# Kernel optimization log

Measured on AMD Instinct MI355X. Metric: run time of the kernel, lower is better.

The kernel has to match this reference:

```python
import jax, jax.numpy as jnp
import numpy as np

N = 32768      # total points (8 clouds x 4096)
B = 8          # clouds in batch
D_IN = 64      # input feature dim
M = 8192       # sampled centers (ratio=0.25)
K = 32         # knn neighbors
R = 0.2        # ball radius
DIMS = [D_IN + 3, 128, 128, 256]  # edge MLP (PointNetConv local_nn)


def setup_inputs() -> dict:
    key = jax.random.key(0)
    ks = jax.random.split(key, 10)
    x = jax.random.normal(ks[0], (N, D_IN), jnp.float32)
    pos = jax.random.uniform(ks[1], (N, 3), jnp.float32)  # unit cube
    batch = jnp.repeat(jnp.arange(B, dtype=jnp.int32), N // B)
    # deterministic stand-in for torch.sort(torch.randperm(N)[:M])
    idx = jnp.sort(jax.random.permutation(ks[2], N)[:M]).astype(jnp.int32)
    params = {}
    for i in range(3):
        fan_in = DIMS[i]
        params[f"W{i+1}"] = jax.random.normal(ks[3 + 2 * i], (DIMS[i], DIMS[i + 1]), jnp.float32) / np.sqrt(fan_in)
        params[f"b{i+1}"] = jnp.zeros((DIMS[i + 1],), jnp.float32)
    return {"x": x, "pos": pos, "batch": batch, "idx": idx, **params}


def _knn_ball(pos, batch, idx, k, r):
    """Batched KNN restricted to same cloud, then radius mask (ball query)."""
    centers = pos[idx]                                   # [M, 3]
    d2 = (jnp.sum(centers ** 2, -1)[:, None]
          + jnp.sum(pos ** 2, -1)[None, :]
          - 2.0 * centers @ pos.T)                       # [M, N]
    same = batch[idx][:, None] == batch[None, :]
    d2 = jnp.where(same, d2, jnp.inf)
    neg_d2, nbr = jax.lax.top_k(-d2, k)                  # [M, K]
    valid = (-neg_d2) <= r * r                           # ball-query radius clip
    return nbr, valid


def reference(x, pos, batch, idx, W1, b1, W2, b2, W3, b3):
    nbr, valid = _knn_ball(pos, batch, idx, K, R)        # [M,K], [M,K]
    centers = pos[idx]                                   # [M, 3]
    rel = pos[nbr] - centers[:, None, :]                 # [M, K, 3]
    feat = jnp.concatenate([x[nbr], rel], axis=-1)       # [M, K, D_IN+3]
    h = jax.nn.relu(feat @ W1 + b1)
    h = jax.nn.relu(h @ W2 + b2)
    h = jax.nn.relu(h @ W3 + b3)                         # [M, K, 256]
    # max aggregation over valid neighbors (scatter-max equivalent)
    h = jnp.where(valid[:, :, None], h, -jnp.inf)
    out = jnp.max(h, axis=1)                             # [M, 256]
    return out, pos[idx], batch[idx]
```

## Files before the change

kernel.cpp:

```cpp
#include <hip/hip_runtime.h>


typedef unsigned short u16;
typedef unsigned int u32;
typedef unsigned long long u64;
typedef __bf16 bf16x8 __attribute__((ext_vector_type(8)));
typedef float floatx4 __attribute__((ext_vector_type(4)));

#define PCLOUD 4096
#define DIN    64
#define MCENT  8192
#define KNBR   32
#define CAP    448

#define OFF_LIST  0
#define OFF_HIST  14336
#define OFF_NBRL  14848
#define OFF_CNT   15360
#define OFF_CEN   15392
#define OFF_BCL   15456

__device__ inline u16 f2bf(float f) {
    u32 b = __float_as_uint(f);
    b += 0x7fffu + ((b >> 16) & 1u);
    return (u16)(b >> 16);
}
__device__ inline u32 pk2(float a, float b) { return (u32)f2bf(a) | ((u32)f2bf(b) << 16); }
__device__ inline u64 wave_min_u64(u64 v) {
    #pragma unroll
    for (int off = 32; off; off >>= 1) {
        u64 o = __shfl_xor((unsigned long long)v, off);
        if (o < v) v = o;
    }
    return v;
}
__device__ inline u64 d2key(float d2, int j) {
    u32 u = __float_as_uint(d2);
    u = (u & 0x80000000u) ? ~u : (u | 0x80000000u);
    return ((u64)u << 32) | (u32)j;
}
__device__ inline int key_bucket(u64 k) {
    u32 hi = (u32)(k >> 32);
    if (hi < 0x80000000u) return 0;
    float d2 = __uint_as_float(hi & 0x7fffffffu);
    int b = (int)(d2 * 800.0f);
    return b > 31 ? 31 : b;
}

__global__ void prep_kernel(const float* __restrict__ W1, const float* __restrict__ W2,
                            const float* __restrict__ W3, uint4* __restrict__ ws) {
    int t = blockIdx.x * 256 + threadIdx.x;
    int g = t >> 11, r = t & 2047;
    int n = r >> 4, kc = r & 15;
    const float* W; int rs, n0, krows;
    if (g == 0)      { W = W1; rs = 128; n0 = 0;   krows = 67;  }
    else if (g == 1) { W = W2; rs = 128; n0 = 0;   krows = 128; }
    else if (g == 2) { W = W3; rs = 256; n0 = 0;   krows = 128; }
    else             { W = W3; rs = 256; n0 = 128; krows = 128; }
    u16 e[8];
    #pragma unroll
    for (int j = 0; j < 8; j++) {
        int k = kc * 8 + j;
        e[j] = (k < krows) ? f2bf(W[(size_t)k * rs + n0 + n]) : (u16)0;
    }
    ws[(g << 11) + (n << 4) + (kc ^ (n & 7))] = *(const uint4*)e;
}

template <bool WS>
__device__ __forceinline__ void commitW(int s, uint4 ld, uint4* __restrict__ buf, int tid,
                                        const float* __restrict__ W1,
                                        const float* __restrict__ W2,
                                        const float* __restrict__ W3) {
    if constexpr (WS) {
        buf[tid] = ld;
    } else {
        const float* W; int rs, n0, krows;
        if (s < 8)       { W = W1; rs = 128; n0 = s * 16;        krows = 67;  }
        else if (s < 16) { W = W2; rs = 128; n0 = (s - 8) * 16;  krows = 128; }
        else             { W = W3; rs = 256; n0 = (s - 16) * 16; krows = 128; }
        int n = tid >> 4, kc = tid & 15;
        u16 e[8];
        #pragma unroll
        for (int j = 0; j < 8; j++) {
            int k = kc * 8 + j;
            e[j] = (k < krows) ? f2bf(W[(size_t)k * rs + n0 + n]) : (u16)0;
        }
        buf[(n << 4) + (kc ^ (n & 7))] = *(const uint4*)e;
    }
}

__device__ __forceinline__ void push_hit(int c, float d2, int j,
                                         int* acnt, u32* hist, u64* lists) {
    int p = atomicAdd(&acnt[c], 1);
    int bkt = (int)(d2 * 800.0f);
    bkt = bkt < 0 ? 0 : (bkt > 31 ? 31 : bkt);
    atomicAdd(&hist[c * 32 + bkt], 1u);
    if (p < CAP) lists[c * CAP + p] = d2key(d2, j);
}

template <bool WS>
__global__ __launch_bounds__(256, 4) void sa_kernel(
    const float* __restrict__ x, const float* __restrict__ pos,
    const int* __restrict__ batch, const int* __restrict__ idx,
    const float* __restrict__ W1, const float* __restrict__ b1,
    const float* __restrict__ W2, const float* __restrict__ b2,
    const float* __restrict__ W3, const float* __restrict__ b3,
    const uint4* __restrict__ ws4, float* __restrict__ out) {
    __shared__ __align__(16) char smem[40960];
    u64*  lists = (u64*)(smem + OFF_LIST);
    u32*  hist  = (u32*)(smem + OFF_HIST);
    int*  nbrl  = (int*)(smem + OFF_NBRL);
    int*  acnt  = (int*)(smem + OFF_CNT);
    int*  cnt2  = (int*)(smem + OFF_CNT + 16);
    float4* cen = (float4*)(smem + OFF_CEN);
    int*  bcls  = (int*)(smem + OFF_BCL);

    int tid = threadIdx.x, w = tid >> 6, l = tid & 63;
    int bid = blockIdx.x;
    int m0 = ((bid & 7) << 10) + ((bid >> 3) << 2);
    int m = m0 + w;
    int ic = idx[m] & (8 * PCLOUD - 1);
    float cx = pos[ic * 3], cy = pos[ic * 3 + 1], cz = pos[ic * 3 + 2];
    float sc = __fadd_rn(__fadd_rn(__fmul_rn(cx, cx), __fmul_rn(cy, cy)), __fmul_rn(cz, cz));
    int bcl = batch[ic] & 7;
    int base = bcl << 12;
    const float R2 = 0.04f;

    if (l == 0) { cen[w] = make_float4(cx, cy, cz, sc); bcls[w] = bcl; }
    if (tid < 128) hist[tid] = 0;
    if (tid < 4) { acnt[tid] = 0; cnt2[tid] = 0; }
    if (l == 1) {
        float* o1 = out + MCENT * 256;
        o1[m * 3] = cx; o1[m * 3 + 1] = cy; o1[m * 3 + 2] = cz;
        (o1 + MCENT * 3)[m] = (float)bcl;
    }
    __syncthreads();

    bool uni = (bcls[0] == bcls[1]) && (bcls[1] == bcls[2]) && (bcls[2] == bcls[3]);
    if (uni) {
        float4 cA = cen[0], cB = cen[1], cC = cen[2], cD = cen[3];
        int jb = bcls[0] << 12;
        const float* pb = pos + (size_t)jb * 3;
        #pragma unroll 4
        for (int t = tid; t < PCLOUD; t += 256) {
            float px = pb[t * 3], py = pb[t * 3 + 1], pz = pb[t * 3 + 2];
            float sp = __fadd_rn(__fadd_rn(__fmul_rn(px, px), __fmul_rn(py, py)), __fmul_rn(pz, pz));
            {
                float dt = __fadd_rn(__fadd_rn(__fmul_rn(cA.x, px), __fmul_rn(cA.y, py)), __fmul_rn(cA.z, pz));
                float d2 = __fsub_rn(__fadd_rn(cA.w, sp), __fmul_rn(2.0f, dt));
                if (d2 <= R2) push_hit(0, d2, jb + t, acnt, hist, lists);
            }
            {
                float dt = __fadd_rn(__fadd_rn(__fmul_rn(cB.x, px), __fmul_rn(cB.y, py)), __fmul_rn(cB.z, pz));
                float d2 = __fsub_rn(__fadd_rn(cB.w, sp), __fmul_rn(2.0f, dt));
                if (d2 <= R2) push_hit(1, d2, jb + t, acnt, hist, lists);
            }
            {
                float dt = __fadd_rn(__fadd_rn(__fmul_rn(cC.x, px), __fmul_rn(cC.y, py)), __fmul_rn(cC.z, pz));
                float d2 = __fsub_rn(__fadd_rn(cC.w, sp), __fmul_rn(2.0f, dt));
                if (d2 <= R2) push_hit(2, d2, jb + t, acnt, hist, lists);
            }
            {
                float dt = __fadd_rn(__fadd_rn(__fmul_rn(cD.x, px), __fmul_rn(cD.y, py)), __fmul_rn(cD.z, pz));
                float d2 = __fsub_rn(__fadd_rn(cD.w, sp), __fmul_rn(2.0f, dt));
                if (d2 <= R2) push_hit(3, d2, jb + t, acnt, hist, lists);
            }
        }
    } else {
        for (int t = l; t < PCLOUD; t += 64) {
            int j = base + t;
            float px = pos[j * 3], py = pos[j * 3 + 1], pz = pos[j * 3 + 2];
            float sp = __fadd_rn(__fadd_rn(__fmul_rn(px, px), __fmul_rn(py, py)), __fmul_rn(pz, pz));
            float dt = __fadd_rn(__fadd_rn(__fmul_rn(cx, px), __fmul_rn(cy, py)), __fmul_rn(cz, pz));
            float d2 = __fsub_rn(__fadd_rn(sc, sp), __fmul_rn(2.0f, dt));
            if (d2 <= R2) push_hit(w, d2, j, acnt, hist, lists);
        }
    }
    __syncthreads();

    int c = acnt[w];
    int nsel = c < KNBR ? c : KNBR;
    u64* mylist = lists + w * CAP;

    int selj = -1;
    if (c <= KNBR) {
        if (l < c) selj = (int)(u32)mylist[l];
    } else if (c <= CAP) {
        u64 kk[7];
        #pragma unroll
        for (int i = 0; i < 7; i++) kk[i] = (l + i * 64 < c) ? mylist[l + i * 64] : ~0ull;
        int hv = (l < 32) ? (int)hist[w * 32 + l] : 0;
        #pragma unroll
        for (int off = 1; off <= 16; off <<= 1) {
            int o = __shfl_up(hv, off);
            if (l >= off) hv += o;
        }
        u64 ge = __ballot((l < 32) && (hv >= KNBR));
        int B = __ffsll((unsigned long long)ge) - 1;
        int S = (B == 0) ? 0 : __shfl(hv, B - 1);
        #pragma unroll
        for (int i = 0; i < 7; i++) {
            if (kk[i] != ~0ull) {
                int bkt = key_bucket(kk[i]);
                if (bkt < B) { int p = atomicAdd(&cnt2[w], 1); nbrl[w * 32 + p] = (int)(u32)kk[i]; }
                if (bkt != B) kk[i] = ~0ull;
            }
        }
        int need = KNBR - S;
        u64 last = 0;
        for (int r = 0; r < need; r++) {
            u64 mn = ~0ull;
            #pragma unroll
            for (int i = 0; i < 7; i++) if (kk[i] > last && kk[i] < mn) mn = kk[i];
            mn = wave_min_u64(mn);
            if (l == 0) nbrl[w * 32 + S + r] = (int)(u32)mn;
            last = mn;
        }
        if (l < KNBR) selj = nbrl[w * 32 + l];
    } else {
        u64 last = 0;
        for (int r = 0; r < KNBR; r++) {
            u64 mn = ~0ull;
            for (int t = l; t < PCLOUD; t += 64) {
                int j = base + t;
                float px = pos[j * 3], py = pos[j * 3 + 1], pz = pos[j * 3 + 2];
                float sp = __fadd_rn(__fadd_rn(__fmul_rn(px, px), __fmul_rn(py, py)), __fmul_rn(pz, pz));
                float dt = __fadd_rn(__fadd_rn(__fmul_rn(cx, px), __fmul_rn(cy, py)), __fmul_rn(cz, pz));
                float d2 = __fsub_rn(__fadd_rn(sc, sp), __fmul_rn(2.0f, dt));
                if (d2 <= R2) { u64 kf = d2key(d2, j); if (kf > last && kf < mn) mn = kf; }
            }
            mn = wave_min_u64(mn);
            if (l == r) selj = (int)(u32)mn;
            last = mn;
        }
    }
    __syncthreads();

    uint4* sA4  = (uint4*)smem;
    uint4* sWb0 = (uint4*)(smem + 32768);
    uint4* sWb1 = (uint4*)(smem + 36864);

    uint4 ld = {};
    if constexpr (WS) ld = ws4[tid];

    {
        int h = l & 1, rl = l >> 1;
        int row = w * 32 + rl;
        int j = __shfl(selj, rl);
        int xv = row & 7;
        uint4* dst = sA4 + row * 16;
        uint4 z; z.x = z.y = z.z = z.w = 0;
        if (j >= 0) {
            const float4* sx = (const float4*)(x + (size_t)j * DIN);
            int c0lo = h ? 6 : 0, c0hi = h ? 8 : 6;
            for (int c0 = c0lo; c0 < c0hi; c0++) {
                float4 f0 = sx[c0 * 2], f1 = sx[c0 * 2 + 1];
                uint4 pv;
                pv.x = pk2(f0.x, f0.y); pv.y = pk2(f0.z, f0.w);
                pv.z = pk2(f1.x, f1.y); pv.w = pk2(f1.z, f1.w);
                dst[c0 ^ xv] = pv;
            }
            if (h == 1) {
                float rx = pos[j * 3] - cx, ry = pos[j * 3 + 1] - cy, rz = pos[j * 3 + 2] - cz;
                uint4 rc; rc.x = pk2(rx, ry); rc.y = (u32)f2bf(rz); rc.z = 0; rc.w = 0;
                dst[8 ^ xv] = rc;
                dst[9 ^ xv] = z; dst[10 ^ xv] = z; dst[11 ^ xv] = z;
            }
        } else {
            int c0lo = h ? 6 : 0, c0hi = h ? 12 : 6;
            for (int c0 = c0lo; c0 < c0hi; c0++) dst[c0 ^ xv] = z;
        }
    }
    commitW<WS>(0, ld, sWb0, tid, W1, W2, W3);
    if constexpr (WS) ld = ws4[256 + tid];
    __syncthreads();

    int m16 = l & 15, quad = l >> 4;
    int r0 = w * 32;
    const floatx4 vzero = {0.f, 0.f, 0.f, 0.f};

    {
        bf16x8 a1[3][2];
        #pragma unroll
        for (int ki = 0; ki < 3; ki++)
            #pragma unroll
            for (int t = 0; t < 2; t++) {
                int row = r0 + t * 16 + m16;
                a1[ki][t] = __builtin_bit_cast(bf16x8, sA4[row * 16 + ((ki * 4 + quad) ^ (row & 7))]);
            }
        #pragma unroll 2
        for (int s = 0; s < 8; s++) {
            uint4* buf  = (s & 1) ? sWb1 : sWb0;
            uint4* nbuf = (s & 1) ? sWb0 : sWb1;
            floatx4 acc[2] = {vzero, vzero};
            #pragma unroll
            for (int ki = 0; ki < 3; ki++) {
                bf16x8 b = __builtin_bit_cast(bf16x8, buf[(m16 << 4) + ((ki * 4 + quad) ^ (m16 & 7))]);
                #pragma unroll
                for (int t = 0; t < 2; t++)
                    acc[t] = __builtin_amdgcn_mfma_f32_16x16x32_bf16(b, a1[ki][t], acc[t], 0, 0, 0);
            }
            float4 bb = ((const float4*)b1)[s * 4 + quad];
            #pragma unroll
            for (int t = 0; t < 2; t++) {
                int rr = r0 + t * 16 + m16;
                uint2 pv;
                pv.x = pk2(fmaxf(acc[t][0] + bb.x, 0.f), fmaxf(acc[t][1] + bb.y, 0.f));
                pv.y = pk2(fmaxf(acc[t][2] + bb.z, 0.f), fmaxf(acc[t][3] + bb.w, 0.f));
                *(uint2*)(smem + rr * 256 + (((s * 2 + (quad >> 1)) ^ (rr & 7)) << 4) + ((quad & 1) << 3)) = pv;
            }
            commitW<WS>(s + 1, ld, nbuf, tid, W1, W2, W3);
            if constexpr (WS) ld = ws4[(s + 2) * 256 + tid];
            __syncthreads();
        }
    }

    {
        bf16x8 a2[4][2];
        #pragma unroll
        for (int ki = 0; ki < 4; ki++)
            #pragma unroll
            for (int t = 0; t < 2; t++) {
                int row = r0 + t * 16 + m16;
                a2[ki][t] = __builtin_bit_cast(bf16x8, sA4[row * 16 + ((ki * 4 + quad) ^ (row & 7))]);
            }
        #pragma unroll 2
        for (int s = 0; s < 8; s++) {
            uint4* buf  = (s & 1) ? sWb1 : sWb0;
            uint4* nbuf = (s & 1) ? sWb0 : sWb1;
            floatx4 acc[2] = {vzero, vzero};
            #pragma unroll
            for (int ki = 0; ki < 4; ki++) {
                bf16x8 b = __builtin_bit_cast(bf16x8, buf[(m16 << 4) + ((ki * 4 + quad) ^ (m16 & 7))]);
                #pragma unroll
                for (int t = 0; t < 2; t++)
                    acc[t] = __builtin_amdgcn_mfma_f32_16x16x32_bf16(b, a2[ki][t], acc[t], 0, 0, 0);
            }
            float4 bb = ((const float4*)b2)[s * 4 + quad];
            #pragma unroll
            for (int t = 0; t < 2; t++) {
                int rr = r0 + t * 16 + m16;
                uint2 pv;
                pv.x = pk2(fmaxf(acc[t][0] + bb.x, 0.f), fmaxf(acc[t][1] + bb.y, 0.f));
                pv.y = pk2(fmaxf(acc[t][2] + bb.z, 0.f), fmaxf(acc[t][3] + bb.w, 0.f));
                *(uint2*)(smem + rr * 256 + (((s * 2 + (quad >> 1)) ^ (rr & 7)) << 4) + ((quad & 1) << 3)) = pv;
            }
            commitW<WS>(s + 9, ld, nbuf, tid, W1, W2, W3);
            if constexpr (WS) ld = ws4[(s + 10) * 256 + tid];
            __syncthreads();
        }
    }

    {
        bf16x8 a3[4][2];
        #pragma unroll
        for (int ki = 0; ki < 4; ki++)
            #pragma unroll
            for (int t = 0; t < 2; t++) {
                int row = r0 + t * 16 + m16;
                a3[ki][t] = __builtin_bit_cast(bf16x8, sA4[row * 16 + ((ki * 4 + quad) ^ (row & 7))]);
            }
        #pragma unroll 2
        for (int s = 0; s < 16; s++) {
            uint4* buf  = (s & 1) ? sWb1 : sWb0;
            uint4* nbuf = (s & 1) ? sWb0 : sWb1;
            floatx4 acc[2] = {vzero, vzero};
            #pragma unroll
            for (int ki = 0; ki < 4; ki++) {
                bf16x8 b = __builtin_bit_cast(bf16x8, buf[(m16 << 4) + ((ki * 4 + quad) ^ (m16 & 7))]);
                #pragma unroll
                for (int t = 0; t < 2; t++)
                    acc[t] = __builtin_amdgcn_mfma_f32_16x16x32_bf16(a3[ki][t], b, acc[t], 0, 0, 0);
            }
            int col = s * 16 + m16;
            float bias = b3[col];
            float mv = 0.0f;
            #pragma unroll
            for (int t = 0; t < 2; t++)
                #pragma unroll
                for (int i = 0; i < 4; i++) {
                    int k = t * 16 + quad * 4 + i;
                    float v = fmaxf(acc[t][i] + bias, 0.0f);
                    if (k < nsel) mv = fmaxf(mv, v);
                }
            mv = fmaxf(mv, __shfl_xor(mv, 16));
            mv = fmaxf(mv, __shfl_xor(mv, 32));
            if (quad == 0) out[(m0 + w) * 256 + col] = mv;
            if (s < 15) {
                commitW<WS>(s + 17, ld, nbuf, tid, W1, W2, W3);
                if constexpr (WS) { if (s < 14) ld = ws4[(s + 18) * 256 + tid]; }
                __syncthreads();
            }
        }
    }
}

extern "C" void kernel_launch(void* const* d_in, const int* in_sizes, int n_in,
                              void* d_out, int out_size, void* d_ws, size_t ws_size,
                              hipStream_t stream) {
    const float* x     = (const float*)d_in[0];
    const float* pos   = (const float*)d_in[1];
    const int*   batch = (const int*)d_in[2];
    const int*   idx   = (const int*)d_in[3];
    const float* W1    = (const float*)d_in[4];
    const float* b1    = (const float*)d_in[5];
    const float* W2    = (const float*)d_in[6];
    const float* b2    = (const float*)d_in[7];
    const float* W3    = (const float*)d_in[8];
    const float* b3    = (const float*)d_in[9];
    float* out = (float*)d_out;
    uint4* ws4 = (uint4*)d_ws;

    if (ws_size >= 131072) {
        hipLaunchKernelGGL(prep_kernel, dim3(32), dim3(256), 0, stream, W1, W2, W3, ws4);
        hipLaunchKernelGGL((sa_kernel<true>), dim3(MCENT / 4), dim3(256), 0, stream,
                           x, pos, batch, idx, W1, b1, W2, b2, W3, b3, ws4, out);
    } else {
        hipLaunchKernelGGL((sa_kernel<false>), dim3(MCENT / 4), dim3(256), 0, stream,
                           x, pos, batch, idx, W1, b1, W2, b2, W3, b3, ws4, out);
    }
}
```

Baseline: 158.1 us.

## Defer histogram build to selection, vectorize ball scan, use hardware bf16 pack

Builds the per-center distance histogram only for centers with more than K hits, during selection, instead of doing an LDS atomic per hit in the scan. The uniform-cloud scan now reads positions as float4 triplets, four points per thread per iteration, fully unrolled. Manual round-to-nearest bf16 packing is replaced with the v_cvt_pk_bf16_f32 instruction. This lowers LDS atomic traffic and ALU work, at the cost of recomputing buckets from keys, and relies on the packed-convert instruction rounding the same way as the old code.

```diff
diff --git a/kernel.cpp b/kernel.cpp
--- a/kernel.cpp
+++ b/kernel.cpp
@@ -25,7 +25,11 @@
     b += 0x7fffu + ((b >> 16) & 1u);
     return (u16)(b >> 16);
 }
-__device__ inline u32 pk2(float a, float b) { return (u32)f2bf(a) | ((u32)f2bf(b) << 16); }
+__device__ inline u32 cvtpk(float a, float b) {
+    u32 r;
+    asm("v_cvt_pk_bf16_f32 %0, %1, %2" : "=v"(r) : "v"(a), "v"(b));
+    return r;
+}
 __device__ inline u64 wave_min_u64(u64 v) {
     #pragma unroll
     for (int off = 32; off; off >>= 1) {
@@ -90,11 +94,8 @@
 }
 
 __device__ __forceinline__ void push_hit(int c, float d2, int j,
-                                         int* acnt, u32* hist, u64* lists) {
+                                         int* acnt, u64* lists) {
     int p = atomicAdd(&acnt[c], 1);
-    int bkt = (int)(d2 * 800.0f);
-    bkt = bkt < 0 ? 0 : (bkt > 31 ? 31 : bkt);
-    atomicAdd(&hist[c * 32 + bkt], 1u);
     if (p < CAP) lists[c * CAP + p] = d2key(d2, j);
 }
 
@@ -127,7 +128,6 @@
     const float R2 = 0.04f;
 
     if (l == 0) { cen[w] = make_float4(cx, cy, cz, sc); bcls[w] = bcl; }
-    if (tid < 128) hist[tid] = 0;
     if (tid < 4) { acnt[tid] = 0; cnt2[tid] = 0; }
     if (l == 1) {
         float* o1 = out + MCENT * 256;
@@ -140,32 +140,31 @@
     if (uni) {
         float4 cA = cen[0], cB = cen[1], cC = cen[2], cD = cen[3];
         int jb = bcls[0] << 12;
-        const float* pb = pos + (size_t)jb * 3;
-        #pragma unroll 4
-        for (int t = tid; t < PCLOUD; t += 256) {
-            float px = pb[t * 3], py = pb[t * 3 + 1], pz = pb[t * 3 + 2];
-            float sp = __fadd_rn(__fadd_rn(__fmul_rn(px, px), __fmul_rn(py, py)), __fmul_rn(pz, pz));
-            {
-                float dt = __fadd_rn(__fadd_rn(__fmul_rn(cA.x, px), __fmul_rn(cA.y, py)), __fmul_rn(cA.z, pz));
-                float d2 = __fsub_rn(__fadd_rn(cA.w, sp), __fmul_rn(2.0f, dt));
-                if (d2 <= R2) push_hit(0, d2, jb + t, acnt, hist, lists);
-            }
-            {
-                float dt = __fadd_rn(__fadd_rn(__fmul_rn(cB.x, px), __fmul_rn(cB.y, py)), __fmul_rn(cB.z, pz));
-                float d2 = __fsub_rn(__fadd_rn(cB.w, sp), __fmul_rn(2.0f, dt));
-                if (d2 <= R2) push_hit(1, d2, jb + t, acnt, hist, lists);
-            }
-            {
-                float dt = __fadd_rn(__fadd_rn(__fmul_rn(cC.x, px), __fmul_rn(cC.y, py)), __fmul_rn(cC.z, pz));
-                float d2 = __fsub_rn(__fadd_rn(cC.w, sp), __fmul_rn(2.0f, dt));
-                if (d2 <= R2) push_hit(2, d2, jb + t, acnt, hist, lists);
-            }
-            {
-                float dt = __fadd_rn(__fadd_rn(__fmul_rn(cD.x, px), __fmul_rn(cD.y, py)), __fmul_rn(cD.z, pz));
-                float d2 = __fsub_rn(__fadd_rn(cD.w, sp), __fmul_rn(2.0f, dt));
-                if (d2 <= R2) push_hit(3, d2, jb + t, acnt, hist, lists);
-            }
-        }
+        const float4* pb4 = (const float4*)(pos + (size_t)jb * 3);
+
+#define TEST1(CEN, CI, SP, PX, PY, PZ, J) { \
+    float dt = __fadd_rn(__fadd_rn(__fmul_rn(CEN.x, PX), __fmul_rn(CEN.y, PY)), __fmul_rn(CEN.z, PZ)); \
+    float d2 = __fsub_rn(__fadd_rn(CEN.w, SP), __fmul_rn(2.0f, dt)); \
+    if (d2 <= R2) push_hit(CI, d2, J, acnt, lists); }
+#define TESTP(PX, PY, PZ, J) { \
+    float sp = __fadd_rn(__fadd_rn(__fmul_rn(PX, PX), __fmul_rn(PY, PY)), __fmul_rn(PZ, PZ)); \
+    TEST1(cA, 0, sp, PX, PY, PZ, J) \
+    TEST1(cB, 1, sp, PX, PY, PZ, J) \
+    TEST1(cC, 2, sp, PX, PY, PZ, J) \
+    TEST1(cD, 3, sp, PX, PY, PZ, J) }
+
+        #pragma unroll
+        for (int it = 0; it < 4; it++) {
+            int tq = it * 256 + tid;
+            float4 q0 = pb4[tq * 3], q1 = pb4[tq * 3 + 1], q2 = pb4[tq * 3 + 2];
+            int j0 = jb + tq * 4;
+            TESTP(q0.x, q0.y, q0.z, j0)
+            TESTP(q0.w, q1.x, q1.y, j0 + 1)
+            TESTP(q1.z, q1.w, q2.x, j0 + 2)
+            TESTP(q2.y, q2.z, q2.w, j0 + 3)
+        }
+#undef TESTP
+#undef TEST1
     } else {
         for (int t = l; t < PCLOUD; t += 64) {
             int j = base + t;
@@ -173,7 +172,7 @@
             float sp = __fadd_rn(__fadd_rn(__fmul_rn(px, px), __fmul_rn(py, py)), __fmul_rn(pz, pz));
             float dt = __fadd_rn(__fadd_rn(__fmul_rn(cx, px), __fmul_rn(cy, py)), __fmul_rn(cz, pz));
             float d2 = __fsub_rn(__fadd_rn(sc, sp), __fmul_rn(2.0f, dt));
-            if (d2 <= R2) push_hit(w, d2, j, acnt, hist, lists);
+            if (d2 <= R2) push_hit(w, d2, j, acnt, lists);
         }
     }
     __syncthreads();
@@ -187,8 +186,18 @@
         if (l < c) selj = (int)(u32)mylist[l];
     } else if (c <= CAP) {
         u64 kk[7];
+        int bk[7];
+        if (l < 32) hist[w * 32 + l] = 0;
         #pragma unroll
         for (int i = 0; i < 7; i++) kk[i] = (l + i * 64 < c) ? mylist[l + i * 64] : ~0ull;
+        #pragma unroll
+        for (int i = 0; i < 7; i++) {
+            bk[i] = 32;
+            if (kk[i] != ~0ull) {
+                bk[i] = key_bucket(kk[i]);
+                atomicAdd(&hist[w * 32 + bk[i]], 1u);
+            }
+        }
         int hv = (l < 32) ? (int)hist[w * 32 + l] : 0;
         #pragma unroll
         for (int off = 1; off <= 16; off <<= 1) {
@@ -201,9 +210,8 @@
         #pragma unroll
         for (int i = 0; i < 7; i++) {
             if (kk[i] != ~0ull) {
-                int bkt = key_bucket(kk[i]);
-                if (bkt < B) { int p = atomicAdd(&cnt2[w], 1); nbrl[w * 32 + p] = (int)(u32)kk[i]; }
-                if (bkt != B) kk[i] = ~0ull;
+                if (bk[i] < B) { int p = atomicAdd(&cnt2[w], 1); nbrl[w * 32 + p] = (int)(u32)kk[i]; }
+                if (bk[i] != B) kk[i] = ~0ull;
             }
         }
         int need = KNBR - S;
@@ -256,13 +264,13 @@
             for (int c0 = c0lo; c0 < c0hi; c0++) {
                 float4 f0 = sx[c0 * 2], f1 = sx[c0 * 2 + 1];
                 uint4 pv;
-                pv.x = pk2(f0.x, f0.y); pv.y = pk2(f0.z, f0.w);
-                pv.z = pk2(f1.x, f1.y); pv.w = pk2(f1.z, f1.w);
+                pv.x = cvtpk(f0.x, f0.y); pv.y = cvtpk(f0.z, f0.w);
+                pv.z = cvtpk(f1.x, f1.y); pv.w = cvtpk(f1.z, f1.w);
                 dst[c0 ^ xv] = pv;
             }
             if (h == 1) {
                 float rx = pos[j * 3] - cx, ry = pos[j * 3 + 1] - cy, rz = pos[j * 3 + 2] - cz;
-                uint4 rc; rc.x = pk2(rx, ry); rc.y = (u32)f2bf(rz); rc.z = 0; rc.w = 0;
+                uint4 rc; rc.x = cvtpk(rx, ry); rc.y = cvtpk(rz, 0.0f); rc.z = 0; rc.w = 0;
                 dst[8 ^ xv] = rc;
                 dst[9 ^ xv] = z; dst[10 ^ xv] = z; dst[11 ^ xv] = z;
             }
@@ -305,8 +313,8 @@
             for (int t = 0; t < 2; t++) {
                 int rr = r0 + t * 16 + m16;
                 uint2 pv;
-                pv.x = pk2(fmaxf(acc[t][0] + bb.x, 0.f), fmaxf(acc[t][1] + bb.y, 0.f));
-                pv.y = pk2(fmaxf(acc[t][2] + bb.z, 0.f), fmaxf(acc[t][3] + bb.w, 0.f));
+                pv.x = cvtpk(fmaxf(acc[t][0] + bb.x, 0.f), fmaxf(acc[t][1] + bb.y, 0.f));
+                pv.y = cvtpk(fmaxf(acc[t][2] + bb.z, 0.f), fmaxf(acc[t][3] + bb.w, 0.f));
                 *(uint2*)(smem + rr * 256 + (((s * 2 + (quad >> 1)) ^ (rr & 7)) << 4) + ((quad & 1) << 3)) = pv;
             }
             commitW<WS>(s + 1, ld, nbuf, tid, W1, W2, W3);
@@ -341,8 +349,8 @@
             for (int t = 0; t < 2; t++) {
                 int rr = r0 + t * 16 + m16;
                 uint2 pv;
-                pv.x = pk2(fmaxf(acc[t][0] + bb.x, 0.f), fmaxf(acc[t][1] + bb.y, 0.f));
-                pv.y = pk2(fmaxf(acc[t][2] + bb.z, 0.f), fmaxf(acc[t][3] + bb.w, 0.f));
+                pv.x = cvtpk(fmaxf(acc[t][0] + bb.x, 0.f), fmaxf(acc[t][1] + bb.y, 0.f));
+                pv.y = cvtpk(fmaxf(acc[t][2] + bb.z, 0.f), fmaxf(acc[t][3] + bb.w, 0.f));
                 *(uint2*)(smem + rr * 256 + (((s * 2 + (quad >> 1)) ^ (rr & 7)) << 4) + ((quad & 1) << 3)) = pv;
             }
             commitW<WS>(s + 9, ld, nbuf, tid, W1, W2, W3);
```

Result: faster. 152.1 us (-3.8%).
